# Performance work log

Measured on AMD Instinct MI355X. Metric: run time of the kernel, lower is better.

The kernel has to match this reference:

```python
import jax, jax.numpy as jnp
import numpy as np

SPINS = (16, 16)
D_FEAT = 1024
H1 = (4096, 4096, 2048)
H2 = (2048, 1)


def _pair_idx(n):
    # Matches: idx_h1 = [i for i in range(n-1) for j in range(n-1-i)]
    #          h2 = concat(h[k:] for k in 1..n-1)  -> all ordered pairs (i, j), i < j
    i = np.repeat(np.arange(n - 1), np.arange(n - 1, 0, -1))
    j = np.concatenate([np.arange(k + 1, n) for k in range(n - 1)])
    return i.astype(np.int32), j.astype(np.int32)


def setup_inputs():
    key = jax.random.key(0)
    ks = jax.random.split(key, 6)

    def w(k, fi, fo, scale):
        return (scale / np.sqrt(fi)).astype(np.float32) * jax.random.normal(k, (fi, fo), jnp.float32)

    d_in = 2 * D_FEAT
    return {
        "h_one": jax.random.normal(ks[0], (sum(SPINS), D_FEAT), jnp.float32),
        "w1_0": w(ks[1], d_in, H1[0], np.float32(np.sqrt(2.0))),
        "b1_0": jnp.zeros((H1[0],), jnp.float32),
        "w1_1": w(ks[2], H1[0], H1[1], np.float32(np.sqrt(2.0))),
        "b1_1": jnp.zeros((H1[1],), jnp.float32),
        # final mlp1 layer scaled so |hidden| ~ 2: keeps the pair-product finite in fp32
        "w1_2": w(ks[3], H1[1], H1[2], np.float32(2.0)),
        "b1_2": jnp.zeros((H1[2],), jnp.float32),
        "w2_0": w(ks[4], H1[2], H2[0], np.float32(1.0)),
        "b2_0": jnp.zeros((H2[0],), jnp.float32),
        "w2_1": w(ks[5], H2[0], H2[1], np.float32(1.0)),
        "b2_1": jnp.zeros((H2[1],), jnp.float32),
    }


def reference(h_one, w1_0, b1_0, w1_1, b1_1, w1_2, b1_2, w2_0, b2_0, w2_1, b2_1):
    def mlp1(x):  # silu hidden layers, linear output
        x = jax.nn.silu(x @ w1_0 + b1_0)
        x = jax.nn.silu(x @ w1_1 + b1_1)
        return x @ w1_2 + b1_2

    def mlp2(x):  # tanh hidden layer, linear scalar output
        x = jnp.tanh(x @ w2_0 + b2_0)
        return x @ w2_1 + b2_1

    sumlogA = jnp.float32(0.0)
    off = 0
    for n in SPINS:  # fixed, small, structurally distinct loop over spin channels
        h = h_one[off:off + n]
        off += n
        ii, jj = _pair_idx(n)  # static numpy indices
        h1, h2 = h[ii], h[jj]  # [P, D] pairwise gathers, P = n*(n-1)/2
        hidden = mlp1(jnp.concatenate([h1, h2], axis=-1)) \
               - mlp1(jnp.concatenate([h2, h1], axis=-1))  # antisymmetric in (h1, h2)
        a = jnp.prod(hidden, axis=0)  # product-reduce over pairs -> [H1[-1]]
        A = mlp2(a)                   # [1]
        sumlogA = sumlogA + jnp.log(jnp.abs(A)).squeeze()
    return sumlogA
```

## Files before the change

### kernel.cpp

```cpp
#include <hip/hip_runtime.h>
#include <hip/hip_bf16.h>
#include <math.h>


typedef __attribute__((ext_vector_type(8))) short short8;
typedef __attribute__((ext_vector_type(4))) float floatx4;

#define AS1 __attribute__((address_space(1)))
#define AS3 __attribute__((address_space(3)))
#define GLD16(g, l) __builtin_amdgcn_global_load_lds((AS1 const unsigned int*)(g), (AS3 unsigned int*)(l), 16, 0, 0)

__device__ __forceinline__ float silu_f(float x) {
    return x / (1.0f + __expf(-x));
}

__device__ __forceinline__ void split2(float x, unsigned short& hi, unsigned short& lo) {
    unsigned u = __float_as_uint(x);
    unsigned r = u + 0x7FFFu + ((u >> 16) & 1u);
    unsigned short h = (unsigned short)(r >> 16);
    float hf = __uint_as_float((unsigned)h << 16);
    float rem = x - hf;
    unsigned u2 = __float_as_uint(rem);
    unsigned r2 = u2 + 0x7FFFu + ((u2 >> 16) & 1u);
    hi = h;
    lo = (unsigned short)(r2 >> 16);
}

__global__ __launch_bounds__(256)
void transpose_split_all(const float* __restrict__ w10, const float* __restrict__ w11,
                         const float* __restrict__ w12, const float* __restrict__ h_one,
                         unsigned short* __restrict__ t10h, unsigned short* __restrict__ t10l,
                         unsigned short* __restrict__ t11h, unsigned short* __restrict__ t11l,
                         unsigned short* __restrict__ t12h, unsigned short* __restrict__ t12l,
                         unsigned short* __restrict__ Hh, unsigned short* __restrict__ Hl) {
    const int t = threadIdx.x;
    int id = blockIdx.x;

    if (id >= 8192) {
        const int base = (id - 8192) * 4096 + t * 16;
        #pragma unroll
        for (int j = 0; j < 4; ++j) {
            float4 v = *(const float4*)&h_one[base + 4 * j];
            ushort4 hv, lv;
            split2(v.x, hv.x, lv.x);
            split2(v.y, hv.y, lv.y);
            split2(v.z, hv.z, lv.z);
            split2(v.w, hv.w, lv.w);
            *(ushort4*)&Hh[base + 4 * j] = hv;
            *(ushort4*)&Hl[base + 4 * j] = lv;
        }
        return;
    }

    const float* W;
    unsigned short *Th, *Tl;
    int K, N, nt, kt;
    if (id < 2048)       { W = w10; Th = t10h; Tl = t10l; K = 2048; N = 4096; nt = id & 63; kt = id >> 6; }
    else if (id < 6144)  { id -= 2048; W = w11; Th = t11h; Tl = t11l; K = 4096; N = 4096; nt = id & 63; kt = id >> 6; }
    else                 { id -= 6144; W = w12; Th = t12h; Tl = t12l; K = 4096; N = 2048; nt = id & 31; kt = id >> 5; }

    const int n0 = nt * 64;
    const int k0 = kt * 64;

    const int wave = t >> 6;
    const int lane = t & 63;
    const int kw = (wave >> 1) * 32 + ((lane >> 3) & 7) * 4;
    const int nw = (wave & 1) * 32 + (lane & 7) * 4;

    const float* src = &W[(size_t)(k0 + kw) * N + n0 + nw];
    float a[4][4];
    #pragma unroll
    for (int r = 0; r < 4; ++r) {
        float4 v = *(const float4*)(src + (size_t)r * N);
        a[r][0] = v.x; a[r][1] = v.y; a[r][2] = v.z; a[r][3] = v.w;
    }

    unsigned short* dh = &Th[(size_t)(n0 + nw) * K + k0 + kw];
    unsigned short* dl = &Tl[(size_t)(n0 + nw) * K + k0 + kw];
    #pragma unroll
    for (int c = 0; c < 4; ++c) {
        ushort4 hv, lv;
        split2(a[0][c], hv.x, lv.x);
        split2(a[1][c], hv.y, lv.y);
        split2(a[2][c], hv.z, lv.z);
        split2(a[3][c], hv.w, lv.w);
        *(ushort4*)(dh + (size_t)c * K) = hv;
        *(ushort4*)(dl + (size_t)c * K) = lv;
    }
}

__global__ __launch_bounds__(256, 2)
void gemm128(const unsigned short* __restrict__ Ah, const unsigned short* __restrict__ Al,
             const unsigned short* __restrict__ Bh, const unsigned short* __restrict__ Bl,
             int K, float* __restrict__ Cpart, int N, int Mtot, int kc)
{
    __shared__ __align__(16) unsigned short As[2][128][32];
    __shared__ __align__(16) unsigned short Bs[2][128][32];

    const int tid  = threadIdx.x;
    const int lane = tid & 63;
    const int wid  = tid >> 6;
    const int n0 = blockIdx.x * 128;
    const int m0 = blockIdx.y * 128;
    const int kbase = blockIdx.z * kc;

    const int srow   = wid * 32 + (lane >> 2);
    const int schunk = (lane & 3) ^ ((srow >> 1) & 3);
    const unsigned short* gA0h = Ah + (size_t)(m0 + srow) * K + kbase + schunk * 8;
    const unsigned short* gA1h = gA0h + (size_t)16 * K;
    const unsigned short* gA0l = Al + (size_t)(m0 + srow) * K + kbase + schunk * 8;
    const unsigned short* gA1l = gA0l + (size_t)16 * K;
    const unsigned short* gB0h = Bh + (size_t)(n0 + srow) * K + kbase + schunk * 8;
    const unsigned short* gB1h = gB0h + (size_t)16 * K;
    const unsigned short* gB0l = Bl + (size_t)(n0 + srow) * K + kbase + schunk * 8;
    const unsigned short* gB1l = gB0l + (size_t)16 * K;
    unsigned short* lA0h = &As[0][wid * 32][0];
    unsigned short* lA1h = &As[0][wid * 32 + 16][0];
    unsigned short* lA0l = &As[1][wid * 32][0];
    unsigned short* lA1l = &As[1][wid * 32 + 16][0];
    unsigned short* lB0h = &Bs[0][wid * 32][0];
    unsigned short* lB1h = &Bs[0][wid * 32 + 16][0];
    unsigned short* lB0l = &Bs[1][wid * 32][0];
    unsigned short* lB1l = &Bs[1][wid * 32 + 16][0];

    const int mhalf = wid >> 1;
    const int nhalf = wid & 1;
    const int lm = lane & 15;
    const int q  = lane >> 4;
    int aoffs[4], boffs[4];
    #pragma unroll
    for (int f = 0; f < 4; ++f) {
        int arow = mhalf * 64 + f * 16 + lm;
        int aslot = q ^ ((arow >> 1) & 3);
        aoffs[f] = arow * 32 + aslot * 8;
        int brow = nhalf * 64 + f * 16 + lm;
        int bslot = q ^ ((brow >> 1) & 3);
        boffs[f] = brow * 32 + bslot * 8;
    }
    const unsigned short* AsF = &As[0][0][0];
    const unsigned short* BsF = &Bs[0][0][0];

    floatx4 acc[4][4];
    #pragma unroll
    for (int ms = 0; ms < 4; ++ms)
        #pragma unroll
        for (int ns = 0; ns < 4; ++ns)
            acc[ms][ns] = (floatx4){0.f, 0.f, 0.f, 0.f};

    const int S = kc >> 5;
    for (int s = 0; s < S; ++s) {
        const int ko = s << 5;
        __syncthreads();
        GLD16(gA0h + ko, lA0h);
        GLD16(gA1h + ko, lA1h);
        GLD16(gA0l + ko, lA0l);
        GLD16(gA1l + ko, lA1l);
        GLD16(gB0h + ko, lB0h);
        GLD16(gB1h + ko, lB1h);
        GLD16(gB0l + ko, lB0l);
        GLD16(gB1l + ko, lB1l);
        __syncthreads();

        short8 afh[4], afl[4], bfh[4], bfl[4];
        #pragma unroll
        for (int f = 0; f < 4; ++f) {
            afh[f] = *(const short8*)(AsF + aoffs[f]);
            afl[f] = *(const short8*)(AsF + 4096 + aoffs[f]);
            bfh[f] = *(const short8*)(BsF + boffs[f]);
            bfl[f] = *(const short8*)(BsF + 4096 + boffs[f]);
        }
        #pragma unroll
        for (int ms = 0; ms < 4; ++ms)
            #pragma unroll
            for (int ns = 0; ns < 4; ++ns)
                acc[ms][ns] = __builtin_amdgcn_mfma_f32_16x16x32_bf16(afh[ms], bfh[ns], acc[ms][ns], 0, 0, 0);
        #pragma unroll
        for (int ms = 0; ms < 4; ++ms)
            #pragma unroll
            for (int ns = 0; ns < 4; ++ns)
                acc[ms][ns] = __builtin_amdgcn_mfma_f32_16x16x32_bf16(afl[ms], bfh[ns], acc[ms][ns], 0, 0, 0);
        #pragma unroll
        for (int ms = 0; ms < 4; ++ms)
            #pragma unroll
            for (int ns = 0; ns < 4; ++ns)
                acc[ms][ns] = __builtin_amdgcn_mfma_f32_16x16x32_bf16(afh[ms], bfl[ns], acc[ms][ns], 0, 0, 0);
    }

    float* Cp = Cpart + (size_t)blockIdx.z * Mtot * N;
    const int lr = (lane >> 4) * 4;
    #pragma unroll
    for (int ms = 0; ms < 4; ++ms)
        #pragma unroll
        for (int ns = 0; ns < 4; ++ns)
            #pragma unroll
            for (int r = 0; r < 4; ++r)
                Cp[(size_t)(m0 + mhalf * 64 + ms * 16 + lr + r) * N + n0 + nhalf * 64 + ns * 16 + lm] = acc[ms][ns][r];
}

__device__ __forceinline__ void load_set(
    const unsigned short* __restrict__ Ah, const unsigned short* __restrict__ Al,
    const unsigned short* __restrict__ Bh, const unsigned short* __restrict__ Bl,
    const unsigned aoff[4], const unsigned boff[4], int koff,
    short8 (&ah)[4], short8 (&al)[4], short8 (&bh)[4], short8 (&bl)[4])
{
    #pragma unroll
    for (int i = 0; i < 4; ++i) {
        ah[i] = *(const short8*)(Ah + aoff[i] + koff);
        al[i] = *(const short8*)(Al + aoff[i] + koff);
        bh[i] = *(const short8*)(Bh + boff[i] + koff);
        bl[i] = *(const short8*)(Bl + boff[i] + koff);
    }
}

__device__ __forceinline__ void mfma_set(
    const short8 (&ah)[4], const short8 (&al)[4],
    const short8 (&bh)[4], const short8 (&bl)[4],
    floatx4 (&acc)[4][4])
{
    #pragma unroll
    for (int ms = 0; ms < 4; ++ms)
        #pragma unroll
        for (int ns = 0; ns < 4; ++ns)
            acc[ms][ns] = __builtin_amdgcn_mfma_f32_16x16x32_bf16(ah[ms], bh[ns], acc[ms][ns], 0, 0, 0);
    #pragma unroll
    for (int ms = 0; ms < 4; ++ms)
        #pragma unroll
        for (int ns = 0; ns < 4; ++ns)
            acc[ms][ns] = __builtin_amdgcn_mfma_f32_16x16x32_bf16(al[ms], bh[ns], acc[ms][ns], 0, 0, 0);
    #pragma unroll
    for (int ms = 0; ms < 4; ++ms)
        #pragma unroll
        for (int ns = 0; ns < 4; ++ns)
            acc[ms][ns] = __builtin_amdgcn_mfma_f32_16x16x32_bf16(ah[ms], bl[ns], acc[ms][ns], 0, 0, 0);
}

__global__ __launch_bounds__(256, 2)
void pq_gemm(const unsigned short* __restrict__ Ah, const unsigned short* __restrict__ Al,
             const unsigned short* __restrict__ Bh0, const unsigned short* __restrict__ Bl0,
             float* __restrict__ PQ)
{
    const int tid  = threadIdx.x;
    const int lane = tid & 63;
    const int wid  = tid >> 6;
    const int n0 = blockIdx.x * 256 + wid * 64;
    const int z  = blockIdx.z;
    const int kbase = (z & 1) * 512;
    const unsigned short* Bh = Bh0 + (z >> 1) * 1024;
    const unsigned short* Bl = Bl0 + (z >> 1) * 1024;
    const int lm = lane & 15;
    const int lk = (lane >> 4) * 8;

    unsigned aoff[4], boff[4];
    #pragma unroll
    for (int i = 0; i < 4; ++i) {
        aoff[i] = (unsigned)(i * 16 + lm) * 1024 + kbase + lk;
        boff[i] = (unsigned)(n0 + i * 16 + lm) * 2048 + kbase + lk;
    }

    floatx4 acc[4][4];
    #pragma unroll
    for (int ms = 0; ms < 4; ++ms)
        #pragma unroll
        for (int ns = 0; ns < 4; ++ns)
            acc[ms][ns] = (floatx4){0.f, 0.f, 0.f, 0.f};

    short8 a0h[4], a0l[4], b0h[4], b0l[4];
    short8 a1h[4], a1l[4], b1h[4], b1l[4];

    load_set(Ah, Al, Bh, Bl, aoff, boff, 0, a0h, a0l, b0h, b0l);
    for (int s = 0; s + 1 < 16; s += 2) {
        load_set(Ah, Al, Bh, Bl, aoff, boff, (s + 1) << 5, a1h, a1l, b1h, b1l);
        mfma_set(a0h, a0l, b0h, b0l, acc);
        if (s + 2 < 16)
            load_set(Ah, Al, Bh, Bl, aoff, boff, (s + 2) << 5, a0h, a0l, b0h, b0l);
        mfma_set(a1h, a1l, b1h, b1l, acc);
    }

    float* Cp = PQ + (size_t)z * 64 * 4096;
    const int lr = (lane >> 4) * 4;
    #pragma unroll
    for (int ms = 0; ms < 4; ++ms)
        #pragma unroll
        for (int ns = 0; ns < 4; ++ns)
            #pragma unroll
            for (int r = 0; r < 4; ++r)
                Cp[(size_t)(ms * 16 + lr + r) * 4096 + n0 + ns * 16 + lm] = acc[ms][ns][r];
}

__global__ __launch_bounds__(256)
void build_y1_kernel(const float* __restrict__ PQ, const float* __restrict__ b1,
                     unsigned short* __restrict__ Y1h, unsigned short* __restrict__ Y1l) {
    const int r = blockIdx.x;
    const int g = r / 240;
    const int rem = r % 240;
    const int o = rem / 120;
    const int p = rem % 120;
    int i = 0, pp = p, cnt = 15;
    while (pp >= cnt) { pp -= cnt; cnt--; i++; }
    const int j = i + 1 + pp;
    const int ai = g * 16 + (o ? j : i);
    const int bi = g * 16 + (o ? i : j);
    const size_t chunk4 = (size_t)64 * 4096 / 4;
    const float4* Pr0 = (const float4*)(PQ + (size_t)ai * 4096);
    const float4* Qr0 = (const float4*)(PQ + (size_t)2 * 64 * 4096 + (size_t)bi * 4096);
    const float4* Br  = (const float4*)b1;
    for (int c = threadIdx.x; c < 1024; c += 256) {
        float4 p0 = Pr0[c], p1 = Pr0[c + chunk4];
        float4 q0 = Qr0[c], q1 = Qr0[c + chunk4];
        float4 bv = Br[c];
        float s0 = silu_f(p0.x + p1.x + q0.x + q1.x + bv.x);
        float s1 = silu_f(p0.y + p1.y + q0.y + q1.y + bv.y);
        float s2 = silu_f(p0.z + p1.z + q0.z + q1.z + bv.z);
        float s3 = silu_f(p0.w + p1.w + q0.w + q1.w + bv.w);
        ushort4 hv, lv;
        split2(s0, hv.x, lv.x);
        split2(s1, hv.y, lv.y);
        split2(s2, hv.z, lv.z);
        split2(s3, hv.w, lv.w);
        *(ushort4*)&Y1h[(size_t)r * 4096 + c * 4] = hv;
        *(ushort4*)&Y1l[(size_t)r * 4096 + c * 4] = lv;
    }
}

__global__ __launch_bounds__(256)
void reduce4_silu_split(const float* __restrict__ Part, const float* __restrict__ bias,
                        unsigned short* __restrict__ Yh, unsigned short* __restrict__ Yl) {
    const size_t idx = (size_t)blockIdx.x * 256 + threadIdx.x;
    const size_t stride4 = (size_t)512 * 4096 / 4;
    const float4* p = (const float4*)Part;
    float4 v0 = p[idx], v1 = p[idx + stride4], v2 = p[idx + 2 * stride4], v3 = p[idx + 3 * stride4];
    const int col = (int)((idx * 4) & 4095);
    float4 b = *(const float4*)&bias[col];
    float s0 = silu_f(v0.x + v1.x + v2.x + v3.x + b.x);
    float s1 = silu_f(v0.y + v1.y + v2.y + v3.y + b.y);
    float s2 = silu_f(v0.z + v1.z + v2.z + v3.z + b.z);
    float s3 = silu_f(v0.w + v1.w + v2.w + v3.w + b.w);
    ushort4 hv, lv;
    split2(s0, hv.x, lv.x);
    split2(s1, hv.y, lv.y);
    split2(s2, hv.z, lv.z);
    split2(s3, hv.w, lv.w);
    *(ushort4*)&Yh[idx * 4] = hv;
    *(ushort4*)&Yl[idx * 4] = lv;
}

__global__ __launch_bounds__(256)
void reduce8_bias(const float* __restrict__ Part, const float* __restrict__ bias,
                  float* __restrict__ Hb) {
    const size_t idx = (size_t)blockIdx.x * 256 + threadIdx.x;
    const size_t stride4 = (size_t)512 * 2048 / 4;
    const float4* p = (const float4*)Part;
    float4 s = p[idx];
    #pragma unroll
    for (int c = 1; c < 8; ++c) {
        float4 v = p[idx + c * stride4];
        s.x += v.x; s.y += v.y; s.z += v.z; s.w += v.w;
    }
    const int col = (int)((idx * 4) & 2047);
    float4 b = *(const float4*)&bias[col];
    s.x += b.x; s.y += b.y; s.z += b.z; s.w += b.w;
    *(float4*)&Hb[idx * 4] = s;
}

__global__ __launch_bounds__(256)
void reduce_prod_kernel(const float* __restrict__ H, float* __restrict__ a_buf) {
    const int g = blockIdx.y;
    const int c = blockIdx.x * 256 + threadIdx.x;
    const float* base = H + (size_t)g * 240 * 2048 + c;
    float prod = 1.0f;
    for (int p = 0; p < 120; ++p) {
        float f = base[(size_t)p * 2048] - base[(size_t)(120 + p) * 2048];
        prod *= f;
    }
    a_buf[g * 2048 + c] = prod;
}

__global__ __launch_bounds__(256)
void mlp2_acc2_kernel(const float* __restrict__ a_buf, const float* __restrict__ W,
                      float* __restrict__ Part2) {
    __shared__ float a0s[256], a1s[256];
    const int kc = blockIdx.y, nc = blockIdx.x, t = threadIdx.x;
    a0s[t] = a_buf[kc * 256 + t];
    a1s[t] = a_buf[2048 + kc * 256 + t];
    __syncthreads();
    const int n = nc * 256 + t;
    const float* Wp = W + (size_t)(kc * 256) * 2048 + n;
    float s0 = 0.f, s1 = 0.f;
    #pragma unroll 8
    for (int kk = 0; kk < 256; ++kk) {
        float w = Wp[(size_t)kk * 2048];
        s0 = fmaf(a0s[kk], w, s0);
        s1 = fmaf(a1s[kk], w, s1);
    }
    Part2[kc * 4096 + n] = s0;
    Part2[kc * 4096 + 2048 + n] = s1;
}

__global__ __launch_bounds__(256)
void finalize_kernel(const float* __restrict__ Part2, const float* __restrict__ b2_0,
                     const float* __restrict__ w2_1, const float* __restrict__ b2_1,
                     float* __restrict__ out) {
    __shared__ float red[256];
    const int tid = threadIdx.x;
    float result = 0.0f;
    for (int g = 0; g < 2; ++g) {
        float s = 0.f;
        for (int n = tid; n < 2048; n += 256) {
            float acc = b2_0[n];
            #pragma unroll
            for (int kc = 0; kc < 8; ++kc)
                acc += Part2[kc * 4096 + g * 2048 + n];
            s += tanhf(acc) * w2_1[n];
        }
        red[tid] = s;
        __syncthreads();
        for (int off = 128; off > 0; off >>= 1) {
            if (tid < off) red[tid] += red[tid + off];
            __syncthreads();
        }
        if (tid == 0) result += logf(fabsf(red[0] + b2_1[0]));
        __syncthreads();
    }
    if (tid == 0) out[0] = result;
}

extern "C" void kernel_launch(void* const* d_in, const int* in_sizes, int n_in,
                              void* d_out, int out_size, void* d_ws, size_t ws_size,
                              hipStream_t stream) {
    const float* h_one = (const float*)d_in[0];
    const float* w1_0  = (const float*)d_in[1];
    const float* b1_0  = (const float*)d_in[2];
    const float* w1_1  = (const float*)d_in[3];
    const float* b1_1  = (const float*)d_in[4];
    const float* w1_2  = (const float*)d_in[5];
    const float* b1_2  = (const float*)d_in[6];
    const float* w2_0  = (const float*)d_in[7];
    const float* b2_0  = (const float*)d_in[8];
    const float* w2_1  = (const float*)d_in[9];
    const float* b2_1  = (const float*)d_in[10];
    float* out = (float*)d_out;

    char* ws = (char*)d_ws;
    unsigned short* W10t_h = (unsigned short*)ws;
    unsigned short* W10t_l = W10t_h + (size_t)4096 * 2048;
    float*          PartL1 = (float*)ws;
    ws += (size_t)4096 * 2048 * 2 * 2;
    unsigned short* W11t_h = (unsigned short*)ws;
    unsigned short* W11t_l = W11t_h + (size_t)4096 * 4096;
    float*          PartL2 = (float*)ws;
    ws += (size_t)4096 * 4096 * 2 * 2;
    unsigned short* W12t_h = (unsigned short*)ws;
    unsigned short* W12t_l = W12t_h + (size_t)2048 * 4096;
    ws += (size_t)2048 * 4096 * 2 * 2;
    unsigned short* Hh  = (unsigned short*)ws;  ws += (size_t)64 * 1024 * 2;
    unsigned short* Hl  = (unsigned short*)ws;  ws += (size_t)64 * 1024 * 2;
    float* PQ  = (float*)ws;                    ws += (size_t)4 * 64 * 4096 * 4;
    unsigned short* Y1h = (unsigned short*)ws;  ws += (size_t)512 * 4096 * 2;
    unsigned short* Y1l = (unsigned short*)ws;  ws += (size_t)512 * 4096 * 2;
    unsigned short* Y2h = (unsigned short*)ws;  ws += (size_t)512 * 4096 * 2;
    unsigned short* Y2l = (unsigned short*)ws;  ws += (size_t)512 * 4096 * 2;
    float* Hb    = (float*)ws;                  ws += (size_t)512 * 2048 * 4;
    float* a_buf = (float*)ws;                  ws += (size_t)2 * 2048 * 4;
    float* Part2 = (float*)ws;                  ws += (size_t)8 * 2 * 2048 * 4;

    transpose_split_all<<<8200, 256, 0, stream>>>(w1_0, w1_1, w1_2, h_one,
                                                  W10t_h, W10t_l, W11t_h, W11t_l,
                                                  W12t_h, W12t_l, Hh, Hl);

    pq_gemm<<<dim3(16, 1, 4), 256, 0, stream>>>(Hh, Hl, W10t_h, W10t_l, PQ);
    build_y1_kernel<<<480, 256, 0, stream>>>(PQ, b1_0, Y1h, Y1l);

    gemm128<<<dim3(32, 4, 4), 256, 0, stream>>>(Y1h, Y1l, W11t_h, W11t_l, 4096,
                                                PartL1, 4096, 512, 1024);
    reduce4_silu_split<<<2048, 256, 0, stream>>>(PartL1, b1_1, Y2h, Y2l);

    gemm128<<<dim3(16, 4, 8), 256, 0, stream>>>(Y2h, Y2l, W12t_h, W12t_l, 4096,
                                                PartL2, 2048, 512, 512);
    reduce8_bias<<<1024, 256, 0, stream>>>(PartL2, b1_2, Hb);

    reduce_prod_kernel<<<dim3(8, 2), 256, 0, stream>>>(Hb, a_buf);
    mlp2_acc2_kernel<<<dim3(8, 8), 256, 0, stream>>>(a_buf, w2_0, Part2);
    finalize_kernel<<<1, 256, 0, stream>>>(Part2, b2_0, w2_1, b2_1, out);
}
```

Before: 383.2 us.

## Store transposed split weights in contiguous 64x64 hi/lo tiles

The transposed bf16 hi/lo weight copies now use a tiled layout: each 64x64 tile takes 8192 contiguous shorts, hi half first and lo half second. The old layout was two separate row-major arrays. The transpose kernel's writes and the B-operand loads in gemm128 and pq_gemm are re-indexed to match. The goal is more contiguous, cache-friendly access for both the transpose stores and the GEMM B-tile loads, at the cost of more complex address arithmetic.

Result: no change. 379.6 us (-1.0%).

```diff
diff --git a/kernel.cpp b/kernel.cpp
--- a/kernel.cpp
+++ b/kernel.cpp
@@ -29,9 +29,8 @@
 __global__ __launch_bounds__(256)
 void transpose_split_all(const float* __restrict__ w10, const float* __restrict__ w11,
                          const float* __restrict__ w12, const float* __restrict__ h_one,
-                         unsigned short* __restrict__ t10h, unsigned short* __restrict__ t10l,
-                         unsigned short* __restrict__ t11h, unsigned short* __restrict__ t11l,
-                         unsigned short* __restrict__ t12h, unsigned short* __restrict__ t12l,
+                         unsigned short* __restrict__ t10, unsigned short* __restrict__ t11,
+                         unsigned short* __restrict__ t12,
                          unsigned short* __restrict__ Hh, unsigned short* __restrict__ Hl) {
     const int t = threadIdx.x;
     int id = blockIdx.x;
@@ -53,11 +52,11 @@
     }
 
     const float* W;
-    unsigned short *Th, *Tl;
-    int K, N, nt, kt;
-    if (id < 2048)       { W = w10; Th = t10h; Tl = t10l; K = 2048; N = 4096; nt = id & 63; kt = id >> 6; }
-    else if (id < 6144)  { id -= 2048; W = w11; Th = t11h; Tl = t11l; K = 4096; N = 4096; nt = id & 63; kt = id >> 6; }
-    else                 { id -= 6144; W = w12; Th = t12h; Tl = t12l; K = 4096; N = 2048; nt = id & 31; kt = id >> 5; }
+    unsigned short* T;
+    int K, N, KT, nt, kt;
+    if (id < 2048)       { W = w10; T = t10; K = 2048; N = 4096; KT = 32; nt = id >> 5; kt = id & 31; }
+    else if (id < 6144)  { id -= 2048; W = w11; T = t11; K = 4096; N = 4096; KT = 64; nt = id >> 6; kt = id & 63; }
+    else                 { id -= 6144; W = w12; T = t12; K = 4096; N = 2048; KT = 64; nt = id >> 6; kt = id & 63; }
 
     const int n0 = nt * 64;
     const int k0 = kt * 64;
@@ -75,8 +74,7 @@
         a[r][0] = v.x; a[r][1] = v.y; a[r][2] = v.z; a[r][3] = v.w;
     }
 
-    unsigned short* dh = &Th[(size_t)(n0 + nw) * K + k0 + kw];
-    unsigned short* dl = &Tl[(size_t)(n0 + nw) * K + k0 + kw];
+    unsigned short* dt = T + (size_t)(nt * KT + kt) * 8192 + (size_t)nw * 64 + kw;
     #pragma unroll
     for (int c = 0; c < 4; ++c) {
         ushort4 hv, lv;
@@ -84,14 +82,14 @@
         split2(a[1][c], hv.y, lv.y);
         split2(a[2][c], hv.z, lv.z);
         split2(a[3][c], hv.w, lv.w);
-        *(ushort4*)(dh + (size_t)c * K) = hv;
-        *(ushort4*)(dl + (size_t)c * K) = lv;
+        *(ushort4*)(dt + c * 64) = hv;
+        *(ushort4*)(dt + 4096 + c * 64) = lv;
     }
 }
 
 __global__ __launch_bounds__(256, 2)
 void gemm128(const unsigned short* __restrict__ Ah, const unsigned short* __restrict__ Al,
-             const unsigned short* __restrict__ Bh, const unsigned short* __restrict__ Bl,
+             const unsigned short* __restrict__ Bt,
              int K, float* __restrict__ Cpart, int N, int Mtot, int kc)
 {
     __shared__ __align__(16) unsigned short As[2][128][32];
@@ -103,6 +101,7 @@
     const int n0 = blockIdx.x * 128;
     const int m0 = blockIdx.y * 128;
     const int kbase = blockIdx.z * kc;
+    const int KT = K >> 6;
 
     const int srow   = wid * 32 + (lane >> 2);
     const int schunk = (lane & 3) ^ ((srow >> 1) & 3);
@@ -110,10 +109,10 @@
     const unsigned short* gA1h = gA0h + (size_t)16 * K;
     const unsigned short* gA0l = Al + (size_t)(m0 + srow) * K + kbase + schunk * 8;
     const unsigned short* gA1l = gA0l + (size_t)16 * K;
-    const unsigned short* gB0h = Bh + (size_t)(n0 + srow) * K + kbase + schunk * 8;
-    const unsigned short* gB1h = gB0h + (size_t)16 * K;
-    const unsigned short* gB0l = Bl + (size_t)(n0 + srow) * K + kbase + schunk * 8;
-    const unsigned short* gB1l = gB0l + (size_t)16 * K;
+    const int brow = n0 + srow;
+    const unsigned short* gB0 = Bt + (size_t)(brow >> 6) * KT * 8192 + (brow & 63) * 64 + schunk * 8;
+    const unsigned short* gB1 = gB0 + 16 * 64;
+
     unsigned short* lA0h = &As[0][wid * 32][0];
     unsigned short* lA1h = &As[0][wid * 32 + 16][0];
     unsigned short* lA0l = &As[1][wid * 32][0];
@@ -133,9 +132,9 @@
         int arow = mhalf * 64 + f * 16 + lm;
         int aslot = q ^ ((arow >> 1) & 3);
         aoffs[f] = arow * 32 + aslot * 8;
-        int brow = nhalf * 64 + f * 16 + lm;
-        int bslot = q ^ ((brow >> 1) & 3);
-        boffs[f] = brow * 32 + bslot * 8;
+        int brw = nhalf * 64 + f * 16 + lm;
+        int bslot = q ^ ((brw >> 1) & 3);
+        boffs[f] = brw * 32 + bslot * 8;
     }
     const unsigned short* AsF = &As[0][0][0];
     const unsigned short* BsF = &Bs[0][0][0];
@@ -150,15 +149,16 @@
     const int S = kc >> 5;
     for (int s = 0; s < S; ++s) {
         const int ko = s << 5;
+        const size_t bko = (size_t)((kbase + ko) >> 6) * 8192 + (ko & 32);
         __syncthreads();
         GLD16(gA0h + ko, lA0h);
         GLD16(gA1h + ko, lA1h);
         GLD16(gA0l + ko, lA0l);
         GLD16(gA1l + ko, lA1l);
-        GLD16(gB0h + ko, lB0h);
-        GLD16(gB1h + ko, lB1h);
-        GLD16(gB0l + ko, lB0l);
-        GLD16(gB1l + ko, lB1l);
+        GLD16(gB0 + bko, lB0h);
+        GLD16(gB1 + bko, lB1h);
+        GLD16(gB0 + bko + 4096, lB0l);
+        GLD16(gB1 + bko + 4096, lB1l);
         __syncthreads();
 
         short8 afh[4], afl[4], bfh[4], bfl[4];
@@ -199,16 +199,16 @@
 
 __device__ __forceinline__ void load_set(
     const unsigned short* __restrict__ Ah, const unsigned short* __restrict__ Al,
-    const unsigned short* __restrict__ Bh, const unsigned short* __restrict__ Bl,
-    const unsigned aoff[4], const unsigned boff[4], int koff,
+    const unsigned short* __restrict__ Bt,
+    const unsigned aoff[4], const size_t boff[4], int koff, size_t bko,
     short8 (&ah)[4], short8 (&al)[4], short8 (&bh)[4], short8 (&bl)[4])
 {
     #pragma unroll
     for (int i = 0; i < 4; ++i) {
         ah[i] = *(const short8*)(Ah + aoff[i] + koff);
         al[i] = *(const short8*)(Al + aoff[i] + koff);
-        bh[i] = *(const short8*)(Bh + boff[i] + koff);
-        bl[i] = *(const short8*)(Bl + boff[i] + koff);
+        bh[i] = *(const short8*)(Bt + boff[i] + bko);
+        bl[i] = *(const short8*)(Bt + boff[i] + bko + 4096);
     }
 }
 
@@ -236,7 +236,7 @@
 
 __global__ __launch_bounds__(256, 2)
 void pq_gemm(const unsigned short* __restrict__ Ah, const unsigned short* __restrict__ Al,
-             const unsigned short* __restrict__ Bh0, const unsigned short* __restrict__ Bl0,
+             const unsigned short* __restrict__ Bt,
              float* __restrict__ PQ)
 {
     const int tid  = threadIdx.x;
@@ -245,16 +245,17 @@
     const int n0 = blockIdx.x * 256 + wid * 64;
     const int z  = blockIdx.z;
     const int kbase = (z & 1) * 512;
-    const unsigned short* Bh = Bh0 + (z >> 1) * 1024;
-    const unsigned short* Bl = Bl0 + (z >> 1) * 1024;
+    const int kzbase = z * 8;
     const int lm = lane & 15;
     const int lk = (lane >> 4) * 8;
 
-    unsigned aoff[4], boff[4];
+    unsigned aoff[4];
+    size_t boff[4];
     #pragma unroll
     for (int i = 0; i < 4; ++i) {
         aoff[i] = (unsigned)(i * 16 + lm) * 1024 + kbase + lk;
-        boff[i] = (unsigned)(n0 + i * 16 + lm) * 2048 + kbase + lk;
+        const int row = n0 + i * 16 + lm;
+        boff[i] = (size_t)(row >> 6) * 32 * 8192 + (row & 63) * 64 + lk;
     }
 
     floatx4 acc[4][4];
@@ -267,12 +268,16 @@
     short8 a0h[4], a0l[4], b0h[4], b0l[4];
     short8 a1h[4], a1l[4], b1h[4], b1l[4];
 
-    load_set(Ah, Al, Bh, Bl, aoff, boff, 0, a0h, a0l, b0h, b0l);
+    auto bko_of = [&](int koff) -> size_t {
+        return (size_t)(kzbase + (koff >> 6)) * 8192 + (koff & 32);
+    };
+
+    load_set(Ah, Al, Bt, aoff, boff, 0, bko_of(0), a0h, a0l, b0h, b0l);
     for (int s = 0; s + 1 < 16; s += 2) {
-        load_set(Ah, Al, Bh, Bl, aoff, boff, (s + 1) << 5, a1h, a1l, b1h, b1l);
+        load_set(Ah, Al, Bt, aoff, boff, (s + 1) << 5, bko_of((s + 1) << 5), a1h, a1l, b1h, b1l);
         mfma_set(a0h, a0l, b0h, b0l, acc);
         if (s + 2 < 16)
-            load_set(Ah, Al, Bh, Bl, aoff, boff, (s + 2) << 5, a0h, a0l, b0h, b0l);
+            load_set(Ah, Al, Bt, aoff, boff, (s + 2) << 5, bko_of((s + 2) << 5), a0h, a0l, b0h, b0l);
         mfma_set(a1h, a1l, b1h, b1l, acc);
     }
 
@@ -441,16 +446,13 @@
     float* out = (float*)d_out;
 
     char* ws = (char*)d_ws;
-    unsigned short* W10t_h = (unsigned short*)ws;
-    unsigned short* W10t_l = W10t_h + (size_t)4096 * 2048;
+    unsigned short* W10t = (unsigned short*)ws;
     float*          PartL1 = (float*)ws;
     ws += (size_t)4096 * 2048 * 2 * 2;
-    unsigned short* W11t_h = (unsigned short*)ws;
-    unsigned short* W11t_l = W11t_h + (size_t)4096 * 4096;
+    unsigned short* W11t = (unsigned short*)ws;
     float*          PartL2 = (float*)ws;
     ws += (size_t)4096 * 4096 * 2 * 2;
-    unsigned short* W12t_h = (unsigned short*)ws;
-    unsigned short* W12t_l = W12t_h + (size_t)2048 * 4096;
+    unsigned short* W12t = (unsigned short*)ws;
     ws += (size_t)2048 * 4096 * 2 * 2;
     unsigned short* Hh  = (unsigned short*)ws;  ws += (size_t)64 * 1024 * 2;
     unsigned short* Hl  = (unsigned short*)ws;  ws += (size_t)64 * 1024 * 2;
@@ -464,17 +466,16 @@
     float* Part2 = (float*)ws;                  ws += (size_t)8 * 2 * 2048 * 4;
 
     transpose_split_all<<<8200, 256, 0, stream>>>(w1_0, w1_1, w1_2, h_one,
-                                                  W10t_h, W10t_l, W11t_h, W11t_l,
-                                                  W12t_h, W12t_l, Hh, Hl);
-
-    pq_gemm<<<dim3(16, 1, 4), 256, 0, stream>>>(Hh, Hl, W10t_h, W10t_l, PQ);
+                                                  W10t, W11t, W12t, Hh, Hl);
+
+    pq_gemm<<<dim3(16, 1, 4), 256, 0, stream>>>(Hh, Hl, W10t, PQ);
     build_y1_kernel<<<480, 256, 0, stream>>>(PQ, b1_0, Y1h, Y1l);
 
-    gemm128<<<dim3(32, 4, 4), 256, 0, stream>>>(Y1h, Y1l, W11t_h, W11t_l, 4096,
+    gemm128<<<dim3(32, 4, 4), 256, 0, stream>>>(Y1h, Y1l, W11t, 4096,
                                                 PartL1, 4096, 512, 1024);
     reduce4_silu_split<<<2048, 256, 0, stream>>>(PartL1, b1_1, Y2h, Y2l);
 
-    gemm128<<<dim3(16, 4, 8), 256, 0, stream>>>(Y2h, Y2l, W12t_h, W12t_l, 4096,
+    gemm128<<<dim3(16, 4, 8), 256, 0, stream>>>(Y2h, Y2l, W12t, 4096,
                                                 PartL2, 2048, 512, 512);
     reduce8_bias<<<1024, 256, 0, stream>>>(PartL2, b1_2, Hb);
 
```
